# Optimization experiments

Hardware: AMD Instinct MI355X
Metric: run time of the kernel (lower is better)

## Reference

```python
import jax, jax.numpy as jnp
import numpy as np

N_PTILES = 4096
MAX_SOURCES = 1
PTILE_SLEN = 53  # odd -> slen == ptile_slen, size_lens is identity
N_BANDS = 1


def setup_inputs() -> dict:
    key = jax.random.key(0)
    k1, k2, k3, k4, k5, k6 = jax.random.split(key, 6)
    shape = (N_PTILES, MAX_SOURCES)
    gal = jax.random.uniform(k1, shape + (7,), dtype=jnp.float32)
    # realistic SIE lens params per _sample_lens_params: b in [5,30], q in (0,1)
    b = jax.random.uniform(k2, shape + (1,), dtype=jnp.float32) * 25.0 + 5.0
    centers = jax.random.normal(k3, shape + (2,), dtype=jnp.float32)
    q = jax.random.uniform(k4, shape + (1,), dtype=jnp.float32) * 0.8 + 0.1
    beta = (jax.random.uniform(k5, shape + (1,), dtype=jnp.float32) - 0.5) * (np.pi / 2)
    ellf = (1.0 - q) / (1.0 + q)
    e1 = ellf * jnp.cos(beta)
    e2 = ellf * jnp.sin(beta)
    lens_params = jnp.concatenate([gal, b, centers, e1, e2], axis=-1)  # [..., 12]
    bools = (jax.random.uniform(k6, shape + (1,), dtype=jnp.float32) < 0.7).astype(jnp.float32)
    return {"lens_params": lens_params, "lensed_galaxy_bools": bools}


def _render_unlensed(gal_p, slen):
    # Differentiable Gaussian stand-in for the (CPU galsim) unlensed source render.
    c = jnp.arange(slen, dtype=jnp.float32) - (slen - 1) / 2.0
    yy, xx = jnp.meshgrid(c, c, indexing="ij")
    flux = gal_p[:, 0] * 1000.0 + 100.0      # [N]
    sigma = gal_p[:, 3] * 3.0 + 1.0          # [N]
    r2 = xx[None] ** 2 + yy[None] ** 2       # [1, S, S]
    s2 = (sigma ** 2)[:, None, None]
    return flux[:, None, None] * jnp.exp(-0.5 * r2 / s2) / (2.0 * np.pi * s2)


def _sie_deflection(x, y, lens_p):
    # x, y: [1, S, S]; lens_p: [N, 5] -> (xg, yg): [N, S, S]
    b, cx, cy, e1, e2 = [lens_p[:, i][:, None, None] for i in range(5)]
    ell = jnp.sqrt(e1 ** 2 + e2 ** 2)
    q = (1.0 - ell) / (1.0 + ell)
    phirad = jnp.arctan(e2 / e1)
    cosp, sinp = jnp.cos(phirad), jnp.sin(phirad)
    xsie = (x - cx) * cosp + (y - cy) * sinp
    ysie = (y - cy) * cosp - (x - cx) * sinp
    r_ell = jnp.sqrt(q * xsie ** 2 + ysie ** 2 / q + 1e-12)
    qfact = jnp.sqrt(1.0 / q - q)
    eps = 0.001
    safe = jnp.maximum(qfact, eps)
    denom = r_ell + (r_ell == 0)
    xtg = jnp.where(qfact >= eps, b / safe * jnp.arctan(safe * xsie / denom), b * xsie / denom)
    ytg = jnp.where(qfact >= eps, b / safe * jnp.arctanh(safe * ysie / denom), b * ysie / denom)
    xg = xtg * cosp - ytg * sinp
    yg = ytg * cosp + xtg * sinp
    return xg, yg


def _bilinear(im, xs, ys):
    # im: [N, S, S]; xs (col coord), ys (row coord): [N, S, S]
    N, S, _ = im.shape
    x0 = jnp.clip(jnp.floor(xs).astype(jnp.int32), 0, S - 1)
    x1 = jnp.clip(jnp.floor(xs).astype(jnp.int32) + 1, 0, S - 1)
    y0 = jnp.clip(jnp.floor(ys).astype(jnp.int32), 0, S - 1)
    y1 = jnp.clip(jnp.floor(ys).astype(jnp.int32) + 1, 0, S - 1)
    flat = im.reshape(N, S * S)

    def g(yi, xi):
        return jnp.take_along_axis(flat, (yi * S + xi).reshape(N, -1), axis=1).reshape(N, S, S)

    x0f, x1f = x0.astype(im.dtype), x1.astype(im.dtype)
    y0f, y1f = y0.astype(im.dtype), y1.astype(im.dtype)
    # weights use the CLIPPED integer corners, matching bilinear_interpolate_numpy
    wa = (x1f - xs) * (y1f - ys)
    wb = (x1f - xs) * (ys - y0f)
    wc = (xs - x0f) * (y1f - ys)
    wd = (xs - x0f) * (ys - y0f)
    return g(y0, x0) * wa + g(y1, x0) * wb + g(y0, x1) * wc + g(y1, x1) * wd


def _forward(lens_params, lensed_galaxy_bools):
    n_ptiles, max_s, P = lens_params.shape
    z = lens_params.reshape(-1, P)
    gal_p, lens_p = z[:, :7], z[:, 7:]
    slen = PTILE_SLEN
    unlensed = _render_unlensed(gal_p, slen)            # [N, S, S]
    # grid exactly as lens_galsim: range [-nx//2, nx//2] over nx points
    nx = slen
    lo = float((-nx) // 2)   # -27 for nx=53
    hi = float(nx // 2)      # 26
    coords = (hi - lo) * jnp.arange(nx, dtype=jnp.float32) / (nx - 1) + lo
    x = jnp.broadcast_to(coords[None, :], (nx, nx))  # varies along columns
    y = jnp.broadcast_to(coords[:, None], (nx, nx))  # varies along rows
    xg, yg = _sie_deflection(x[None], y[None], lens_p)
    shift = float(nx // 2)
    lensed = _bilinear(unlensed, x[None] - xg + shift, y[None] - yg + shift)
    out = lensed.reshape(n_ptiles, max_s, N_BANDS, slen, slen)
    # render-all + mask is equivalent to the zeros-init + boolean-fill + final mask
    return out * lensed_galaxy_bools[..., None, None]


def reference(lens_params, lensed_galaxy_bools):
    return _forward(lens_params, lensed_galaxy_bools)
```

## Files before the change

kernel.cpp:

```cpp
#include <hip/hip_runtime.h>
#include <math.h>

#define SLEN 53
#define NPIX (SLEN * SLEN)
#define NPARAM 12

__device__ __forceinline__ float fast_atan(float u) {
    float t = __builtin_fabsf(u);
    float rin = __builtin_amdgcn_rcpf(t);
    bool big = t > 1.0f;
    float w = big ? rin : t;
    bool mid = w > 0.4142135624f;
    float w2 = (w - 1.0f) * __builtin_amdgcn_rcpf(w + 1.0f);
    float x = mid ? w2 : w;
    float z = x * x;
    float p = ((8.05374449538e-2f * z - 1.38776856032e-1f) * z
               + 1.99777106478e-1f) * z - 3.33329491539e-1f;
    float r = __builtin_fmaf(p * z, x, x);
    r = mid ? r + 0.78539816339744831f : r;
    r = big ? 1.57079632679489662f - r : r;
    return __builtin_copysignf(r, u);
}

__device__ __forceinline__ float fast_atanh(float v) {
    float a = __builtin_fabsf(v);
    float r = 0.34657359027997264f *
              (__builtin_amdgcn_logf(1.0f + a) - __builtin_amdgcn_logf(1.0f - a));
    return __builtin_copysignf(r, v);
}

__global__ __launch_bounds__(256) void lgtd_kernel(
    const float* __restrict__ lens_params,
    const float* __restrict__ bools,
    float* __restrict__ out)
{
    const int tile = blockIdx.x;
    float* outp = out + (size_t)tile * NPIX;

    const float bl = bools[tile];
    if (bl == 0.0f) {
        for (int idx = threadIdx.x; idx < NPIX; idx += blockDim.x)
            outp[idx] = 0.0f;
        return;
    }

    const float* p = lens_params + tile * NPARAM;
    const float flux  = p[0] * 1000.0f + 100.0f;
    const float sigma = p[3] * 3.0f + 1.0f;
    const float s2    = sigma * sigma;
    const float A     = bl * flux / (6.28318530717958647692f * s2);
    const float nh2   = -0.5f / s2 * 1.44269504088896340736f;
    const float b  = p[7];
    const float cx = p[8], cy = p[9];
    const float e1 = p[10], e2 = p[11];
    const float ell    = sqrtf(e1 * e1 + e2 * e2);
    const float q      = (1.0f - ell) / (1.0f + ell);
    const float qinv   = 1.0f / q;
    const float phirad = atanf(e2 / e1);
    const float cosp   = cosf(phirad);
    const float sinp   = sinf(phirad);
    const float qfact  = sqrtf(qinv - q);
    const float eps    = 0.001f;
    const float safe   = fmaxf(qfact, eps);
    const float bos    = b / safe;
    const bool  main_branch = (qfact >= eps);

    for (int idx = threadIdx.x; idx < NPIX; idx += blockDim.x) {
        const int i = idx / SLEN;
        const int j = idx - i * SLEN;
        const float xc = 53.0f * (float)j / 52.0f - 27.0f;
        const float yc = 53.0f * (float)i / 52.0f - 27.0f;

        const float dx = xc - cx, dy = yc - cy;
        const float xsie = dx * cosp + dy * sinp;
        const float ysie = dy * cosp - dx * sinp;
        const float arg = q * xsie * xsie + qinv * ysie * ysie + 1e-12f;
        const float rcp_r = __builtin_amdgcn_rsqf(arg);
        float xtg, ytg;
        if (main_branch) {
            xtg = bos * fast_atan(safe * xsie * rcp_r);
            ytg = bos * fast_atanh(safe * ysie * rcp_r);
        } else {
            xtg = b * xsie * rcp_r;
            ytg = b * ysie * rcp_r;
        }
        const float xg = xtg * cosp - ytg * sinp;
        const float yg = ytg * cosp + xtg * sinp;

        const float xs = (xc - xg) + 26.0f;
        const float ys = (yc - yg) + 26.0f;
        const float fx = floorf(xs), fy = floorf(ys);
        const int x0i = (int)fx, y0i = (int)fy;
        const int x0 = min(max(x0i,     0), SLEN - 1);
        const int x1 = min(max(x0i + 1, 0), SLEN - 1);
        const int y0 = min(max(y0i,     0), SLEN - 1);
        const int y1 = min(max(y0i + 1, 0), SLEN - 1);
        const float x0f = (float)x0, x1f = (float)x1;
        const float y0f = (float)y0, y1f = (float)y1;
        const float wa = (x1f - xs) * (y1f - ys);
        const float wb = (x1f - xs) * (ys  - y0f);
        const float wc = (xs - x0f) * (y1f - ys);
        const float wd = (xs - x0f) * (ys  - y0f);

        const float cx0 = x0f - 26.0f, cx1 = x1f - 26.0f;
        const float cy0 = y0f - 26.0f, cy1 = y1f - 26.0f;
        const float sx0 = cx0 * cx0, sx1 = cx1 * cx1;
        const float sy0 = cy0 * cy0, sy1 = cy1 * cy1;
        const float g00 = __builtin_amdgcn_exp2f(nh2 * (sx0 + sy0));
        const float g10 = __builtin_amdgcn_exp2f(nh2 * (sx0 + sy1));
        const float g01 = __builtin_amdgcn_exp2f(nh2 * (sx1 + sy0));
        const float g11 = __builtin_amdgcn_exp2f(nh2 * (sx1 + sy1));

        outp[idx] = A * (g00 * wa + g10 * wb + g01 * wc + g11 * wd);
    }
}

extern "C" void kernel_launch(void* const* d_in, const int* in_sizes, int n_in,
                              void* d_out, int out_size, void* d_ws, size_t ws_size,
                              hipStream_t stream) {
    const float* lens  = (const float*)d_in[0];
    const float* bools = (const float*)d_in[1];
    float* out = (float*)d_out;
    const int n_tiles = in_sizes[1];
    lgtd_kernel<<<n_tiles, 256, 0, stream>>>(lens, bools, out);
}
```

Before: 100.3 us.

## Factor separable Gaussian bilinear sample into per-tile 1D exp tables

Because the Gaussian is separable, the bilinear sample becomes the product of two 1D interpolations. Each interpolation reads a 53-entry shared-memory table of exp values computed once per tile, replacing four exp2 calls per pixel with four LDS reads. Pixel coordinates also come from a shared table, and the pixel loop is fully unrolled with a compile-time trip count. The trade-off is an added __syncthreads, LDS gathers at data-dependent indices, and slightly different floating-point rounding.

```diff
diff --git a/kernel.cpp b/kernel.cpp
--- a/kernel.cpp
+++ b/kernel.cpp
@@ -4,6 +4,8 @@
 #define SLEN 53
 #define NPIX (SLEN * SLEN)
 #define NPARAM 12
+#define BLK 256
+#define NITER ((NPIX + BLK - 1) / BLK)
 
 __device__ __forceinline__ float fast_atan(float u) {
     float t = __builtin_fabsf(u);
@@ -29,18 +31,21 @@
     return __builtin_copysignf(r, v);
 }
 
-__global__ __launch_bounds__(256) void lgtd_kernel(
+__global__ __launch_bounds__(BLK) void lgtd_kernel(
     const float* __restrict__ lens_params,
     const float* __restrict__ bools,
     float* __restrict__ out)
 {
     const int tile = blockIdx.x;
     float* outp = out + (size_t)tile * NPIX;
+    const int tid = threadIdx.x;
 
     const float bl = bools[tile];
     if (bl == 0.0f) {
-        for (int idx = threadIdx.x; idx < NPIX; idx += blockDim.x)
-            outp[idx] = 0.0f;
+        int idx = tid;
+        #pragma unroll
+        for (int it = 0; it < NITER; ++it, idx += BLK)
+            if (it < NITER - 1 || idx < NPIX) outp[idx] = 0.0f;
         return;
     }
 
@@ -65,11 +70,24 @@
     const float bos    = b / safe;
     const bool  main_branch = (qfact >= eps);
 
-    for (int idx = threadIdx.x; idx < NPIX; idx += blockDim.x) {
+    __shared__ float Ctab[SLEN];
+    __shared__ float Etab[SLEN];
+    if (tid < SLEN) {
+        const float kf = (float)tid;
+        Ctab[tid] = 53.0f * kf / 52.0f - 27.0f;
+        const float d = kf - 26.0f;
+        Etab[tid] = __builtin_amdgcn_exp2f(nh2 * (d * d));
+    }
+    __syncthreads();
+
+    int idx = tid;
+    #pragma unroll
+    for (int it = 0; it < NITER; ++it, idx += BLK) {
+        if (it == NITER - 1 && idx >= NPIX) break;
         const int i = idx / SLEN;
         const int j = idx - i * SLEN;
-        const float xc = 53.0f * (float)j / 52.0f - 27.0f;
-        const float yc = 53.0f * (float)i / 52.0f - 27.0f;
+        const float xc = Ctab[j];
+        const float yc = Ctab[i];
 
         const float dx = xc - cx, dy = yc - cy;
         const float xsie = dx * cosp + dy * sinp;
@@ -89,29 +107,17 @@
 
         const float xs = (xc - xg) + 26.0f;
         const float ys = (yc - yg) + 26.0f;
-        const float fx = floorf(xs), fy = floorf(ys);
-        const int x0i = (int)fx, y0i = (int)fy;
+        const int x0i = (int)floorf(xs), y0i = (int)floorf(ys);
         const int x0 = min(max(x0i,     0), SLEN - 1);
         const int x1 = min(max(x0i + 1, 0), SLEN - 1);
         const int y0 = min(max(y0i,     0), SLEN - 1);
         const int y1 = min(max(y0i + 1, 0), SLEN - 1);
         const float x0f = (float)x0, x1f = (float)x1;
         const float y0f = (float)y0, y1f = (float)y1;
-        const float wa = (x1f - xs) * (y1f - ys);
-        const float wb = (x1f - xs) * (ys  - y0f);
-        const float wc = (xs - x0f) * (y1f - ys);
-        const float wd = (xs - x0f) * (ys  - y0f);
 
-        const float cx0 = x0f - 26.0f, cx1 = x1f - 26.0f;
-        const float cy0 = y0f - 26.0f, cy1 = y1f - 26.0f;
-        const float sx0 = cx0 * cx0, sx1 = cx1 * cx1;
-        const float sy0 = cy0 * cy0, sy1 = cy1 * cy1;
-        const float g00 = __builtin_amdgcn_exp2f(nh2 * (sx0 + sy0));
-        const float g10 = __builtin_amdgcn_exp2f(nh2 * (sx0 + sy1));
-        const float g01 = __builtin_amdgcn_exp2f(nh2 * (sx1 + sy0));
-        const float g11 = __builtin_amdgcn_exp2f(nh2 * (sx1 + sy1));
-
-        outp[idx] = A * (g00 * wa + g10 * wb + g01 * wc + g11 * wd);
+        const float Fx = (x1f - xs) * Etab[x0] + (xs - x0f) * Etab[x1];
+        const float Fy = (y1f - ys) * Etab[y0] + (ys - y0f) * Etab[y1];
+        outp[idx] = A * Fx * Fy;
     }
 }
 
@@ -122,5 +128,5 @@
     const float* bools = (const float*)d_in[1];
     float* out = (float*)d_out;
     const int n_tiles = in_sizes[1];
-    lgtd_kernel<<<n_tiles, 256, 0, stream>>>(lens, bools, out);
+    lgtd_kernel<<<n_tiles, BLK, 0, stream>>>(lens, bools, out);
 }
```

Measured after the change: 88.07 us. 1.14x faster.
